# Kernel tuning notes

Measured on AMD Instinct MI355X. Metric: run time of the kernel, lower is better.

Reference implementation:

```python
import jax, jax.numpy as jnp
import numpy as np

EPS = 1e-5

def _conv3x3(x, w, b):
    y = jax.lax.conv_general_dilated(x, w, window_strides=(1, 1),
                                     padding=((1, 1), (1, 1)),
                                     dimension_numbers=('NCHW', 'OIHW', 'NCHW'))
    return y + b[None, :, None, None]

def _bilinear_gather(x, py, px):
    # x: [B,C,H,W]; py,px: [B,K,H,W] absolute sampling coords; zero outside image (DCN convention).
    B, C, H, W = x.shape
    Kk = py.shape[1]
    y0 = jnp.floor(py)
    x0 = jnp.floor(px)
    ly = py - y0
    lx = px - x0
    y0i = y0.astype(jnp.int32)
    x0i = x0.astype(jnp.int32)
    xf = x.reshape(B, C, H * W)

    def gather(yi, xi):
        valid = (yi >= 0) & (yi < H) & (xi >= 0) & (xi < W)
        idx = (jnp.clip(yi, 0, H - 1) * W + jnp.clip(xi, 0, W - 1)).reshape(B, -1)
        g = jax.vmap(lambda xb, ib: xb[:, ib])(xf, idx).reshape(B, C, Kk, H, W)
        return g * valid[:, None].astype(x.dtype)

    v00 = gather(y0i, x0i)
    v01 = gather(y0i, x0i + 1)
    v10 = gather(y0i + 1, x0i)
    v11 = gather(y0i + 1, x0i + 1)
    ly = ly[:, None]
    lx = lx[:, None]
    return (v00 * (1 - ly) * (1 - lx) + v01 * (1 - ly) * lx
            + v10 * ly * (1 - lx) + v11 * ly * lx)

def _shift_forward(x, w_off, b_off, w_conv, b_conv, gamma, beta, run_mean, run_var):
    B, C, H, W = x.shape
    om = _conv3x3(x, w_off, b_off)              # [B,27,H,W] offset/mask predictor
    dy = om[:, 0:18:2]                          # [B,9,H,W] per-tap y offsets
    dx = om[:, 1:18:2]                          # [B,9,H,W] per-tap x offsets
    mask = jax.nn.sigmoid(om[:, 18:27])         # [B,9,H,W] modulation (DCNv2)
    kk = jnp.arange(3, dtype=x.dtype) - 1.0     # kernel tap offsets for 3x3, dilation 1
    ky = jnp.repeat(kk, 3)                      # [9]
    kx = jnp.tile(kk, 3)                        # [9]
    hh = jnp.arange(H, dtype=x.dtype)
    ww = jnp.arange(W, dtype=x.dtype)
    py = hh[None, None, :, None] + ky[None, :, None, None] + dy
    px = ww[None, None, None, :] + kx[None, :, None, None] + dx
    s = _bilinear_gather(x, py, px) * mask[:, None]   # [B,C,9,H,W]
    Co = w_conv.shape[0]
    y = jnp.einsum('bckhw,ock->bohw', s, w_conv.reshape(Co, C, 9))
    y = y + b_conv[None, :, None, None]
    # BatchNorm2d (inference) + ReLU, then residual add
    inv = jax.lax.rsqrt(run_var + EPS)
    y = (y - run_mean[None, :, None, None]) * (inv * gamma)[None, :, None, None] + beta[None, :, None, None]
    y = jax.nn.relu(y)
    return x + y

def setup_inputs():
    key = jax.random.key(0)
    ks = jax.random.split(key, 3)
    B, C, H, W = 2, 256, 96, 96
    x = jax.random.normal(ks[0], (B, C, H, W), dtype=jnp.float32)
    w_off = jax.random.normal(ks[1], (27, C, 3, 3), dtype=jnp.float32) * 0.01
    b_off = jnp.zeros((27,), dtype=jnp.float32)
    w_conv = jax.random.normal(ks[2], (C, C, 3, 3), dtype=jnp.float32) * 0.02
    b_conv = jnp.zeros((C,), dtype=jnp.float32)
    gamma = jnp.ones((C,), dtype=jnp.float32)
    beta = jnp.zeros((C,), dtype=jnp.float32)
    run_mean = jnp.zeros((C,), dtype=jnp.float32)
    run_var = jnp.ones((C,), dtype=jnp.float32)
    return {"x": x, "w_off": w_off, "b_off": b_off, "w_conv": w_conv,
            "b_conv": b_conv, "gamma": gamma, "beta": beta,
            "run_mean": run_mean, "run_var": run_var}

def reference(x, w_off, b_off, w_conv, b_conv, gamma, beta, run_mean, run_var):
    return _shift_forward(x, w_off, b_off, w_conv, b_conv, gamma, beta, run_mean, run_var)
```

## Files before the change

kernel.cpp:

```cpp
#include <hip/hip_runtime.h>
#include <hip/hip_bf16.h>

#define H_ 96
#define W_ 96
#define HW_ 9216
#define C_ 256
#define B_ 2
#define KO_ 27
#define NPX_ 18432
#define EPS_ 1e-5f

typedef unsigned short u16;
typedef unsigned short ushort8 __attribute__((ext_vector_type(8)));
typedef short short8v __attribute__((ext_vector_type(8)));
typedef float float4v __attribute__((ext_vector_type(4)));

__device__ __forceinline__ float b2f(u16 u) {
    return __uint_as_float(((unsigned int)u) << 16);
}
__device__ __forceinline__ u16 f2b(float f) {
    __hip_bfloat16 h = __float2bfloat16(f);
    union { __hip_bfloat16 h; u16 u; } cv; cv.h = h; return cv.u;
}
__device__ __forceinline__ unsigned int pack2(float a, float b) {
    union { __hip_bfloat162 h; unsigned int u; } cv;
    cv.h = __float22bfloat162_rn(make_float2(a, b));
    return cv.u;
}
__device__ __forceinline__ void glds16(const u16* g, u16* l) {
    __builtin_amdgcn_global_load_lds(
        (const __attribute__((address_space(1))) void*)g,
        (__attribute__((address_space(3))) void*)l, 16, 0, 0);
}

__global__ __launch_bounds__(256) void prep_w_kernel(
    const float* __restrict__ w_conv, const float* __restrict__ w_off,
    const float* __restrict__ b_conv,
    const float* __restrict__ gamma, const float* __restrict__ beta,
    const float* __restrict__ rmean, const float* __restrict__ rvar,
    float* __restrict__ AB, u16* __restrict__ WQ, u16* __restrict__ WO)
{
    if (blockIdx.x == 0) {
        int o = threadIdx.x;
        float sc = gamma[o] * rsqrtf(rvar[o] + EPS_);
        AB[o] = sc;
        AB[256 + o] = beta[o] + (b_conv[o] - rmean[o]) * sc;
    }
    if (blockIdx.x < 2304) {
        int idx = blockIdx.x * 256 + threadIdx.x;
        int ch = idx >> 13;
        int o  = (idx >> 5) & 255;
        int cpa = idx & 31;
        int cp  = cpa ^ ((o & 3) << 3);
        int c  = ((ch & 7) << 5) + cp;
        int k  = ch >> 3;
        WQ[idx] = f2b(w_conv[(o * C_ + c) * 9 + k]);
    } else {
        int j = (blockIdx.x - 2304) * 256 + threadIdx.x;
        int ch = j >> 10;
        int o  = (j >> 5) & 31;
        int cp = j & 31;
        int c  = ((ch & 7) << 5) + cp;
        int k  = ch >> 3;
        WO[j] = (o < KO_) ? f2b(w_off[(o * C_ + c) * 9 + k]) : (u16)0;
    }
}

__global__ __launch_bounds__(256) void xt_kernel(const float* __restrict__ x,
                                                 u16* __restrict__ XT)
{
    __shared__ u16 ls[32][100];
    int h  = blockIdx.x;
    int cg = blockIdx.y & 7;
    int b  = blockIdx.y >> 3;
    int c0 = cg * 32;
    for (int e = threadIdx.x; e < 32 * W_; e += 256) {
        int ci = e / W_, w = e % W_;
        ls[ci][w] = f2b(x[((b * C_ + c0 + ci) * H_ + h) * W_ + w]);
    }
    __syncthreads();
    for (int e = threadIdx.x; e < 32 * W_; e += 256) {
        int w = e >> 5, ci = e & 31;
        XT[((b * H_ + h) * W_ + w) * C_ + c0 + ci] = ls[ci][w];
    }
}

__global__ __launch_bounds__(256) void offsets_kernel(
    const u16* __restrict__ XT, const u16* __restrict__ WO,
    const float* __restrict__ b_off, float* __restrict__ OFF)
{
    __shared__ float red[4][32][16];

    const int tid = threadIdx.x;
    const int b  = blockIdx.y;
    const int p0 = blockIdx.x * 16;
    const int h  = p0 / W_;
    const int w0 = p0 % W_;

    const int wave = tid >> 6;
    const int lane = tid & 63;
    const int quad = lane >> 4;
    const int l15  = lane & 15;

    {
        const int pw = w0 + l15;
        float4v acc0 = float4v{0.f,0.f,0.f,0.f};
        float4v acc1 = float4v{0.f,0.f,0.f,0.f};
        int basec = 0; bool vld = true; int curtap = -1;
        auto set_tap = [&](int tap) {
            int py  = h + tap / 3 - 1;
            int pxl = pw + tap % 3 - 1;
            vld = ((unsigned)py < (unsigned)H_) && ((unsigned)pxl < (unsigned)W_);
            int pyc = min(max(py, 0), H_ - 1);
            int pxc = min(max(pxl, 0), W_ - 1);
            basec = ((b * H_ + pyc) * W_ + pxc) * C_ + quad * 8;
        };
        auto bload = [&](int c32) -> ushort8 {
            ushort8 v = *(const ushort8*)(XT + basec + (c32 & 7) * 32);
#pragma unroll
            for (int j = 0; j < 8; j++) v[j] = vld ? v[j] : (u16)0;
            return v;
        };
        const int c0 = wave * 18, c1 = c0 + 18;
        curtap = c0 >> 3;
        set_tap(curtap);
        ushort8 bq = bload(c0);
        short8v wa = *(const short8v*)(WO + c0 * 1024 + l15 * 32 + quad * 8);
        short8v wb = *(const short8v*)(WO + c0 * 1024 + l15 * 32 + quad * 8 + 512);
        for (int i = c0; i < c1; ++i) {
            ushort8 bc = bq;
            short8v wac = wa, wbc = wb;
            int nx = i + 1;
            if (nx < c1) {
                int t = nx >> 3;
                if (t != curtap) { set_tap(t); curtap = t; }
                bq = bload(nx);
                wa = *(const short8v*)(WO + nx * 1024 + l15 * 32 + quad * 8);
                wb = *(const short8v*)(WO + nx * 1024 + l15 * 32 + quad * 8 + 512);
            }
            union { ushort8 u; short8v s; } cb; cb.u = bc;
            acc0 = __builtin_amdgcn_mfma_f32_16x16x32_bf16(wac, cb.s, acc0, 0, 0, 0);
            acc1 = __builtin_amdgcn_mfma_f32_16x16x32_bf16(wbc, cb.s, acc1, 0, 0, 0);
        }
#pragma unroll
        for (int r = 0; r < 4; ++r) {
            red[wave][quad * 4 + r][l15]      = acc0[r];
            red[wave][16 + quad * 4 + r][l15] = acc1[r];
        }
    }
    __syncthreads();
    const int n_base = b * HW_ + p0;
#pragma unroll
    for (int rep = 0; rep < 2; ++rep) {
        int o  = (tid >> 4) + rep * 16;
        int px = tid & 15;
        if (o < KO_) {
            float v = red[0][o][px] + red[1][o][px] + red[2][o][px] + red[3][o][px]
                    + b_off[o];
            OFF[(size_t)(n_base + px) * 32 + o] =
                (o < 18) ? v : 1.f / (1.f + expf(-v));
        }
    }
}

__global__ __launch_bounds__(256) void fused_kernel(
    const float* __restrict__ x, const u16* __restrict__ XT,
    const float* __restrict__ OFF, const u16* __restrict__ WQ,
    const float* __restrict__ AB, float* __restrict__ out)
{
    __shared__ __align__(16) u16 sA[16384];
    __shared__ __align__(16) u16 sB[2048];
    __shared__ float offv[32][32];

    const int tid = threadIdx.x;
    const int wave = tid >> 6;
    const int lane = tid & 63;
    const int quad = lane >> 4;
    const int l15  = lane & 15;
    const int qx   = (quad ^ (l15 & 3)) << 3;

    const int bid = blockIdx.x;
    const int swz = (bid & 7) * 72 + (bid >> 3);
    const int n0  = swz * 32;
    const int b   = n0 / HW_;
    const int p0  = n0 - b * HW_;
    const int h   = p0 / W_;
    const int w0  = p0 % W_;

    {
        int px = tid >> 3, q4 = (tid & 7) * 4;
        float4 v = *(const float4*)(OFF + (size_t)(n0 + px) * 32 + q4);
        *(float4*)&offv[px][q4] = v;
    }
    __syncthreads();

    float4v acc[4][2];
#pragma unroll
    for (int i = 0; i < 4; i++)
#pragma unroll
        for (int jj = 0; jj < 2; jj++)
            acc[i][jj] = float4v{0.f, 0.f, 0.f, 0.f};

    const int le8 = lane * 8;
    const int wo  = wave * 64;

    const int ppx = tid >> 3;
    const int pj  = tid & 7;
    const int sboff = (pj >> 2) * 1024 + ppx * 32
                    + (((pj & 3) ^ (ppx & 3)) << 3);

    float fn0, fn1, fn2, fn3;
    int a00, a01, a10, a11;

    auto tap_setup = [&](int tap) {
        float dy = offv[ppx][2 * tap];
        float dx = offv[ppx][2 * tap + 1];
        float m  = offv[ppx][18 + tap];
        float py  = (float)(h + tap / 3 - 1) + dy;
        float pxx = (float)(w0 + ppx + tap % 3 - 1) + dx;
        float y0f = floorf(py), x0f = floorf(pxx);
        float ly = py - y0f, lx = pxx - x0f;
        int y0 = (int)y0f, x0i = (int)x0f;
        int y1 = y0 + 1, x1 = x0i + 1;
        bool vy0 = (unsigned)y0 < (unsigned)H_;
        bool vy1 = (unsigned)y1 < (unsigned)H_;
        bool vx0 = (unsigned)x0i < (unsigned)W_;
        bool vx1 = (unsigned)x1 < (unsigned)W_;
        fn0 = (vy0 && vx0) ? (1.f - ly) * (1.f - lx) * m : 0.f;
        fn1 = (vy0 && vx1) ? (1.f - ly) * lx * m : 0.f;
        fn2 = (vy1 && vx0) ? ly * (1.f - lx) * m : 0.f;
        fn3 = (vy1 && vx1) ? ly * lx * m : 0.f;
        int y0c = min(max(y0, 0), H_ - 1), y1c = min(max(y1, 0), H_ - 1);
        int x0c = min(max(x0i, 0), W_ - 1), x1c = min(max(x1, 0), W_ - 1);
        a00 = ((b * H_ + y0c) * W_ + x0c) * C_;
        a01 = ((b * H_ + y0c) * W_ + x1c) * C_;
        a10 = ((b * H_ + y1c) * W_ + x0c) * C_;
        a11 = ((b * H_ + y1c) * W_ + x1c) * C_;
    };

    tap_setup(0);
    float fc0 = fn0, fc1 = fn1, fc2 = fn2, fc3 = fn3;
    ushort8 gc00 = *(const ushort8*)(XT + a00 + pj * 8);
    ushort8 gc01 = *(const ushort8*)(XT + a01 + pj * 8);
    ushort8 gc10 = *(const ushort8*)(XT + a10 + pj * 8);
    ushort8 gc11 = *(const ushort8*)(XT + a11 + pj * 8);
#pragma unroll
    for (int i = 0; i < 8; ++i) {
        int unit = i * 4 + wave;
        int cc = unit >> 4;
        glds16(WQ + (size_t)cc * 8192 + (unit & 15) * 512 + le8,
               &sA[unit * 512]);
    }
    ushort8 gn00{}, gn01{}, gn10{}, gn11{};

#pragma unroll 4
    for (int ch = 0; ch < 36; ++ch) {
        {
            float v[8];
#pragma unroll
            for (int t = 0; t < 8; t++)
                v[t] = fc0 * b2f(gc00[t]) + fc1 * b2f(gc01[t])
                     + fc2 * b2f(gc10[t]) + fc3 * b2f(gc11[t]);
            uint4 sv;
            sv.x = pack2(v[0], v[1]);
            sv.y = pack2(v[2], v[3]);
            sv.z = pack2(v[4], v[5]);
            sv.w = pack2(v[6], v[7]);
            *(uint4*)&sB[sboff] = sv;
        }
        asm volatile("s_waitcnt vmcnt(0) lgkmcnt(0)" ::: "memory");
        __builtin_amdgcn_s_barrier();

        short8v af[2][4], bfr[2][2];
#pragma unroll
        for (int cc = 0; cc < 2; ++cc) {
#pragma unroll
            for (int mt = 0; mt < 4; ++mt)
                af[cc][mt] = *(const short8v*)
                    &sA[cc * 8192 + (wo + mt * 16 + l15) * 32 + qx];
#pragma unroll
            for (int nt = 0; nt < 2; ++nt)
                bfr[cc][nt] = *(const short8v*)
                    &sB[cc * 1024 + (nt * 16 + l15) * 32 + qx];
        }
        asm volatile("s_waitcnt lgkmcnt(0)" ::: "memory");
        __builtin_amdgcn_s_barrier();

        if (ch < 35) {
            const int chn = ch + 1, tapn = chn >> 2, qn = chn & 3;
            if (qn == 0) tap_setup(tapn);
            const int cb = qn * 64 + pj * 8;
            gn00 = *(const ushort8*)(XT + a00 + cb);
            gn01 = *(const ushort8*)(XT + a01 + cb);
            gn10 = *(const ushort8*)(XT + a10 + cb);
            gn11 = *(const ushort8*)(XT + a11 + cb);
#pragma unroll
            for (int i = 0; i < 8; ++i) {
                int unit = i * 4 + wave;
                int cc = unit >> 4;
                glds16(WQ + (size_t)(tapn * 8 + qn * 2 + cc) * 8192
                          + (unit & 15) * 512 + le8,
                       &sA[unit * 512]);
            }
        }
        __builtin_amdgcn_s_setprio(1);
#pragma unroll
        for (int cc = 0; cc < 2; ++cc)
#pragma unroll
            for (int mt = 0; mt < 4; ++mt)
#pragma unroll
                for (int nt = 0; nt < 2; ++nt)
                    acc[mt][nt] = __builtin_amdgcn_mfma_f32_16x16x32_bf16(
                        af[cc][mt], bfr[cc][nt], acc[mt][nt], 0, 0, 0);
        __builtin_amdgcn_s_setprio(0);
        gc00 = gn00; gc01 = gn01; gc10 = gn10; gc11 = gn11;
        fc0 = fn0; fc1 = fn1; fc2 = fn2; fc3 = fn3;
    }

    const float* Ao = AB;
    const float* Bo = AB + 256;
#pragma unroll
    for (int mt = 0; mt < 4; mt++) {
#pragma unroll
        for (int nt = 0; nt < 2; nt++) {
            int pix = p0 + nt * 16 + l15;
#pragma unroll
            for (int r = 0; r < 4; r++) {
                int o = wo + mt * 16 + quad * 4 + r;
                float v = acc[mt][nt][r] * Ao[o] + Bo[o];
                v = fmaxf(v, 0.f);
                int gi = (b * C_ + o) * HW_ + pix;
                out[gi] = x[gi] + v;
            }
        }
    }
}

extern "C" void kernel_launch(void* const* d_in, const int* in_sizes, int n_in,
                              void* d_out, int out_size, void* d_ws, size_t ws_size,
                              hipStream_t stream)
{
    (void)in_sizes; (void)n_in; (void)out_size; (void)ws_size;
    const float* x      = (const float*)d_in[0];
    const float* w_off  = (const float*)d_in[1];
    const float* b_off  = (const float*)d_in[2];
    const float* w_conv = (const float*)d_in[3];
    const float* b_conv = (const float*)d_in[4];
    const float* gamma  = (const float*)d_in[5];
    const float* beta   = (const float*)d_in[6];
    const float* rmean  = (const float*)d_in[7];
    const float* rvar   = (const float*)d_in[8];
    float* out = (float*)d_out;

    float* ws = (float*)d_ws;
    float* AB = ws;
    u16* WQ = (u16*)(AB + 512);
    u16* WO = WQ + 589824;
    u16* XT = WO + 73728;
    float* OFF = (float*)(XT + 4718592);

    prep_w_kernel<<<2592, 256, 0, stream>>>(w_conv, w_off, b_conv, gamma, beta,
                                            rmean, rvar, AB, WQ, WO);
    xt_kernel<<<dim3(96, 16), 256, 0, stream>>>(x, XT);
    offsets_kernel<<<dim3(576, 2), 256, 0, stream>>>(XT, WO, b_off, OFF);
    fused_kernel<<<576, 256, 0, stream>>>(x, XT, OFF, WQ, AB, out);
}
```

Measured before the change: 177.6 us.

## Fuse offset predictor into main kernel and merge prep launches; load weights directly

```diff
diff --git a/kernel.cpp b/kernel.cpp
--- a/kernel.cpp
+++ b/kernel.cpp
@@ -12,6 +12,7 @@
 
 typedef unsigned short u16;
 typedef unsigned short ushort8 __attribute__((ext_vector_type(8)));
+typedef unsigned short ushort4v __attribute__((ext_vector_type(4)));
 typedef short short8v __attribute__((ext_vector_type(8)));
 typedef float float4v __attribute__((ext_vector_type(4)));
 
@@ -27,157 +28,77 @@
     cv.h = __float22bfloat162_rn(make_float2(a, b));
     return cv.u;
 }
-__device__ __forceinline__ void glds16(const u16* g, u16* l) {
-    __builtin_amdgcn_global_load_lds(
-        (const __attribute__((address_space(1))) void*)g,
-        (__attribute__((address_space(3))) void*)l, 16, 0, 0);
-}
-
-__global__ __launch_bounds__(256) void prep_w_kernel(
+
+__global__ __launch_bounds__(256) void prep_kernel(
+    const float* __restrict__ x,
     const float* __restrict__ w_conv, const float* __restrict__ w_off,
     const float* __restrict__ b_conv,
     const float* __restrict__ gamma, const float* __restrict__ beta,
     const float* __restrict__ rmean, const float* __restrict__ rvar,
-    float* __restrict__ AB, u16* __restrict__ WQ, u16* __restrict__ WO)
+    float* __restrict__ AB, u16* __restrict__ WQ, u16* __restrict__ WO,
+    u16* __restrict__ XT)
 {
-    if (blockIdx.x == 0) {
-        int o = threadIdx.x;
-        float sc = gamma[o] * rsqrtf(rvar[o] + EPS_);
-        AB[o] = sc;
-        AB[256 + o] = beta[o] + (b_conv[o] - rmean[o]) * sc;
-    }
-    if (blockIdx.x < 2304) {
-        int idx = blockIdx.x * 256 + threadIdx.x;
+    __shared__ u16 ls[32][100];
+    const int bx = blockIdx.x;
+    if (bx < 2304) {
+        if (bx == 0) {
+            int o = threadIdx.x;
+            float sc = gamma[o] * rsqrtf(rvar[o] + EPS_);
+            AB[o] = sc;
+            AB[256 + o] = beta[o] + (b_conv[o] - rmean[o]) * sc;
+        }
+        int idx = bx * 256 + threadIdx.x;
         int ch = idx >> 13;
         int o  = (idx >> 5) & 255;
-        int cpa = idx & 31;
-        int cp  = cpa ^ ((o & 3) << 3);
+        int cp = idx & 31;
         int c  = ((ch & 7) << 5) + cp;
         int k  = ch >> 3;
         WQ[idx] = f2b(w_conv[(o * C_ + c) * 9 + k]);
-    } else {
-        int j = (blockIdx.x - 2304) * 256 + threadIdx.x;
+    } else if (bx < 2592) {
+        int j = (bx - 2304) * 256 + threadIdx.x;
         int ch = j >> 10;
         int o  = (j >> 5) & 31;
         int cp = j & 31;
         int c  = ((ch & 7) << 5) + cp;
         int k  = ch >> 3;
         WO[j] = (o < KO_) ? f2b(w_off[(o * C_ + c) * 9 + k]) : (u16)0;
-    }
-}
-
-__global__ __launch_bounds__(256) void xt_kernel(const float* __restrict__ x,
-                                                 u16* __restrict__ XT)
+    } else {
+        int bid = bx - 2592;
+        int h  = bid % 96;
+        int by = bid / 96;
+        int cg = by & 7;
+        int b  = by >> 3;
+        int c0 = cg * 32;
+        for (int e = threadIdx.x; e < 32 * W_; e += 256) {
+            int ci = e / W_, w = e % W_;
+            ls[ci][w] = f2b(x[((b * C_ + c0 + ci) * H_ + h) * W_ + w]);
+        }
+        __syncthreads();
+        for (int u = threadIdx.x; u < 768; u += 256) {
+            int g4 = u & 7, w = u >> 3;
+            ushort4v v;
+#pragma unroll
+            for (int t = 0; t < 4; t++) v[t] = ls[g4 * 4 + t][w];
+            *(ushort4v*)&XT[((b * H_ + h) * W_ + w) * C_ + c0 + g4 * 4] = v;
+        }
+    }
+}
+
+__global__ __launch_bounds__(256) void fused_kernel(
+    const float* __restrict__ x, const u16* __restrict__ XT,
+    const u16* __restrict__ WO, const float* __restrict__ b_off,
+    const u16* __restrict__ WQ, const float* __restrict__ AB,
+    float* __restrict__ out)
 {
-    __shared__ u16 ls[32][100];
-    int h  = blockIdx.x;
-    int cg = blockIdx.y & 7;
-    int b  = blockIdx.y >> 3;
-    int c0 = cg * 32;
-    for (int e = threadIdx.x; e < 32 * W_; e += 256) {
-        int ci = e / W_, w = e % W_;
-        ls[ci][w] = f2b(x[((b * C_ + c0 + ci) * H_ + h) * W_ + w]);
-    }
-    __syncthreads();
-    for (int e = threadIdx.x; e < 32 * W_; e += 256) {
-        int w = e >> 5, ci = e & 31;
-        XT[((b * H_ + h) * W_ + w) * C_ + c0 + ci] = ls[ci][w];
-    }
-}
-
-__global__ __launch_bounds__(256) void offsets_kernel(
-    const u16* __restrict__ XT, const u16* __restrict__ WO,
-    const float* __restrict__ b_off, float* __restrict__ OFF)
-{
-    __shared__ float red[4][32][16];
-
-    const int tid = threadIdx.x;
-    const int b  = blockIdx.y;
-    const int p0 = blockIdx.x * 16;
-    const int h  = p0 / W_;
-    const int w0 = p0 % W_;
-
+    __shared__ float red[4][2][32][17];
+    __shared__ __align__(16) u16 sB[2048];
+    __shared__ float offv[32][36];
+
+    const int tid  = threadIdx.x;
     const int wave = tid >> 6;
     const int lane = tid & 63;
     const int quad = lane >> 4;
     const int l15  = lane & 15;
-
-    {
-        const int pw = w0 + l15;
-        float4v acc0 = float4v{0.f,0.f,0.f,0.f};
-        float4v acc1 = float4v{0.f,0.f,0.f,0.f};
-        int basec = 0; bool vld = true; int curtap = -1;
-        auto set_tap = [&](int tap) {
-            int py  = h + tap / 3 - 1;
-            int pxl = pw + tap % 3 - 1;
-            vld = ((unsigned)py < (unsigned)H_) && ((unsigned)pxl < (unsigned)W_);
-            int pyc = min(max(py, 0), H_ - 1);
-            int pxc = min(max(pxl, 0), W_ - 1);
-            basec = ((b * H_ + pyc) * W_ + pxc) * C_ + quad * 8;
-        };
-        auto bload = [&](int c32) -> ushort8 {
-            ushort8 v = *(const ushort8*)(XT + basec + (c32 & 7) * 32);
-#pragma unroll
-            for (int j = 0; j < 8; j++) v[j] = vld ? v[j] : (u16)0;
-            return v;
-        };
-        const int c0 = wave * 18, c1 = c0 + 18;
-        curtap = c0 >> 3;
-        set_tap(curtap);
-        ushort8 bq = bload(c0);
-        short8v wa = *(const short8v*)(WO + c0 * 1024 + l15 * 32 + quad * 8);
-        short8v wb = *(const short8v*)(WO + c0 * 1024 + l15 * 32 + quad * 8 + 512);
-        for (int i = c0; i < c1; ++i) {
-            ushort8 bc = bq;
-            short8v wac = wa, wbc = wb;
-            int nx = i + 1;
-            if (nx < c1) {
-                int t = nx >> 3;
-                if (t != curtap) { set_tap(t); curtap = t; }
-                bq = bload(nx);
-                wa = *(const short8v*)(WO + nx * 1024 + l15 * 32 + quad * 8);
-                wb = *(const short8v*)(WO + nx * 1024 + l15 * 32 + quad * 8 + 512);
-            }
-            union { ushort8 u; short8v s; } cb; cb.u = bc;
-            acc0 = __builtin_amdgcn_mfma_f32_16x16x32_bf16(wac, cb.s, acc0, 0, 0, 0);
-            acc1 = __builtin_amdgcn_mfma_f32_16x16x32_bf16(wbc, cb.s, acc1, 0, 0, 0);
-        }
-#pragma unroll
-        for (int r = 0; r < 4; ++r) {
-            red[wave][quad * 4 + r][l15]      = acc0[r];
-            red[wave][16 + quad * 4 + r][l15] = acc1[r];
-        }
-    }
-    __syncthreads();
-    const int n_base = b * HW_ + p0;
-#pragma unroll
-    for (int rep = 0; rep < 2; ++rep) {
-        int o  = (tid >> 4) + rep * 16;
-        int px = tid & 15;
-        if (o < KO_) {
-            float v = red[0][o][px] + red[1][o][px] + red[2][o][px] + red[3][o][px]
-                    + b_off[o];
-            OFF[(size_t)(n_base + px) * 32 + o] =
-                (o < 18) ? v : 1.f / (1.f + expf(-v));
-        }
-    }
-}
-
-__global__ __launch_bounds__(256) void fused_kernel(
-    const float* __restrict__ x, const u16* __restrict__ XT,
-    const float* __restrict__ OFF, const u16* __restrict__ WQ,
-    const float* __restrict__ AB, float* __restrict__ out)
-{
-    __shared__ __align__(16) u16 sA[16384];
-    __shared__ __align__(16) u16 sB[2048];
-    __shared__ float offv[32][32];
-
-    const int tid = threadIdx.x;
-    const int wave = tid >> 6;
-    const int lane = tid & 63;
-    const int quad = lane >> 4;
-    const int l15  = lane & 15;
-    const int qx   = (quad ^ (l15 & 3)) << 3;
 
     const int bid = blockIdx.x;
     const int swz = (bid & 7) * 72 + (bid >> 3);
@@ -188,9 +109,82 @@
     const int w0  = p0 % W_;
 
     {
-        int px = tid >> 3, q4 = (tid & 7) * 4;
-        float4 v = *(const float4*)(OFF + (size_t)(n0 + px) * 32 + q4);
-        *(float4*)&offv[px][q4] = v;
+        float4v oa[2][2];
+#pragma unroll
+        for (int ph = 0; ph < 2; ph++)
+#pragma unroll
+            for (int hh = 0; hh < 2; hh++)
+                oa[ph][hh] = float4v{0.f, 0.f, 0.f, 0.f};
+
+        int basec0 = 0, basec1 = 0; bool vld0 = true, vld1 = true;
+        auto oset = [&](int tap) {
+            int py = h + tap / 3 - 1;
+            bool vy = (unsigned)py < (unsigned)H_;
+            int pyc = min(max(py, 0), H_ - 1);
+            int rowb = (b * H_ + pyc) * W_;
+            {
+                int pxl = w0 + l15 + tap % 3 - 1;
+                vld0 = vy && ((unsigned)pxl < (unsigned)W_);
+                basec0 = (rowb + min(max(pxl, 0), W_ - 1)) * C_ + quad * 8;
+            }
+            {
+                int pxl = w0 + 16 + l15 + tap % 3 - 1;
+                vld1 = vy && ((unsigned)pxl < (unsigned)W_);
+                basec1 = (rowb + min(max(pxl, 0), W_ - 1)) * C_ + quad * 8;
+            }
+        };
+        auto bld0 = [&](int c32) -> ushort8 {
+            ushort8 v = *(const ushort8*)(XT + basec0 + (c32 & 7) * 32);
+#pragma unroll
+            for (int j = 0; j < 8; j++) v[j] = vld0 ? v[j] : (u16)0;
+            return v;
+        };
+        auto bld1 = [&](int c32) -> ushort8 {
+            ushort8 v = *(const ushort8*)(XT + basec1 + (c32 & 7) * 32);
+#pragma unroll
+            for (int j = 0; j < 8; j++) v[j] = vld1 ? v[j] : (u16)0;
+            return v;
+        };
+        const int i0 = wave * 18, i1 = i0 + 18;
+        int curtap = i0 >> 3;
+        oset(curtap);
+        ushort8 b0 = bld0(i0), b1 = bld1(i0);
+        short8v wa = *(const short8v*)(WO + i0 * 1024 + l15 * 32 + quad * 8);
+        short8v wb = *(const short8v*)(WO + i0 * 1024 + l15 * 32 + quad * 8 + 512);
+        for (int i = i0; i < i1; ++i) {
+            ushort8 c0v = b0, c1v = b1;
+            short8v wac = wa, wbc = wb;
+            int nx = i + 1;
+            if (nx < i1) {
+                int t = nx >> 3;
+                if (t != curtap) { oset(t); curtap = t; }
+                b0 = bld0(nx); b1 = bld1(nx);
+                wa = *(const short8v*)(WO + nx * 1024 + l15 * 32 + quad * 8);
+                wb = *(const short8v*)(WO + nx * 1024 + l15 * 32 + quad * 8 + 512);
+            }
+            union { ushort8 u; short8v s; } u0, u1; u0.u = c0v; u1.u = c1v;
+            oa[0][0] = __builtin_amdgcn_mfma_f32_16x16x32_bf16(wac, u0.s, oa[0][0], 0, 0, 0);
+            oa[0][1] = __builtin_amdgcn_mfma_f32_16x16x32_bf16(wbc, u0.s, oa[0][1], 0, 0, 0);
+            oa[1][0] = __builtin_amdgcn_mfma_f32_16x16x32_bf16(wac, u1.s, oa[1][0], 0, 0, 0);
+            oa[1][1] = __builtin_amdgcn_mfma_f32_16x16x32_bf16(wbc, u1.s, oa[1][1], 0, 0, 0);
+        }
+#pragma unroll
+        for (int r = 0; r < 4; ++r) {
+            red[wave][0][quad * 4 + r][l15]      = oa[0][0][r];
+            red[wave][0][16 + quad * 4 + r][l15] = oa[0][1][r];
+            red[wave][1][quad * 4 + r][l15]      = oa[1][0][r];
+            red[wave][1][16 + quad * 4 + r][l15] = oa[1][1][r];
+        }
+    }
+    __syncthreads();
+    for (int u = tid; u < 1024; u += 256) {
+        int px = u & 31, o = u >> 5;
+        if (o < KO_) {
+            int ph = px >> 4, pp = px & 15;
+            float v = red[0][ph][o][pp] + red[1][ph][o][pp]
+                    + red[2][ph][o][pp] + red[3][ph][o][pp] + b_off[o];
+            offv[px][o] = (o < 18) ? v : 1.f / (1.f + expf(-v));
+        }
     }
     __syncthreads();
 
@@ -201,15 +195,13 @@
         for (int jj = 0; jj < 2; jj++)
             acc[i][jj] = float4v{0.f, 0.f, 0.f, 0.f};
 
-    const int le8 = lane * 8;
     const int wo  = wave * 64;
-
     const int ppx = tid >> 3;
     const int pj  = tid & 7;
-    const int sboff = (pj >> 2) * 1024 + ppx * 32
-                    + (((pj & 3) ^ (ppx & 3)) << 3);
-
-    float fn0, fn1, fn2, fn3;
+    const int sboff = (pj >> 2) * 1024 + ppx * 32 + (((pj & 3) ^ (ppx & 3)) << 3);
+    const int bslot = (quad ^ (l15 & 3)) << 3;
+
+    float fc0, fc1, fc2, fc3, fn0, fn1, fn2, fn3;
     int a00, a01, a10, a11;
 
     auto tap_setup = [&](int tap) {
@@ -239,22 +231,26 @@
     };
 
     tap_setup(0);
-    float fc0 = fn0, fc1 = fn1, fc2 = fn2, fc3 = fn3;
+    fc0 = fn0; fc1 = fn1; fc2 = fn2; fc3 = fn3;
     ushort8 gc00 = *(const ushort8*)(XT + a00 + pj * 8);
     ushort8 gc01 = *(const ushort8*)(XT + a01 + pj * 8);
     ushort8 gc10 = *(const ushort8*)(XT + a10 + pj * 8);
     ushort8 gc11 = *(const ushort8*)(XT + a11 + pj * 8);
-#pragma unroll
-    for (int i = 0; i < 8; ++i) {
-        int unit = i * 4 + wave;
-        int cc = unit >> 4;
-        glds16(WQ + (size_t)cc * 8192 + (unit & 15) * 512 + le8,
-               &sA[unit * 512]);
-    }
     ushort8 gn00{}, gn01{}, gn10{}, gn11{};
 
-#pragma unroll 4
+#pragma unroll 1
     for (int ch = 0; ch < 36; ++ch) {
+        const int tap = ch >> 2, q = ch & 3;
+
+        short8v af[2][4];
+        const u16* wq0 = WQ + (size_t)(tap * 8 + q * 2) * 8192
+                       + (wo + l15) * 32 + quad * 8;
+#pragma unroll
+        for (int cc = 0; cc < 2; ++cc)
+#pragma unroll
+            for (int mt = 0; mt < 4; ++mt)
+                af[cc][mt] = *(const short8v*)(wq0 + cc * 8192 + mt * 512);
+
         {
             float v[8];
 #pragma unroll
@@ -268,23 +264,6 @@
             sv.w = pack2(v[6], v[7]);
             *(uint4*)&sB[sboff] = sv;
         }
-        asm volatile("s_waitcnt vmcnt(0) lgkmcnt(0)" ::: "memory");
-        __builtin_amdgcn_s_barrier();
-
-        short8v af[2][4], bfr[2][2];
-#pragma unroll
-        for (int cc = 0; cc < 2; ++cc) {
-#pragma unroll
-            for (int mt = 0; mt < 4; ++mt)
-                af[cc][mt] = *(const short8v*)
-                    &sA[cc * 8192 + (wo + mt * 16 + l15) * 32 + qx];
-#pragma unroll
-            for (int nt = 0; nt < 2; ++nt)
-                bfr[cc][nt] = *(const short8v*)
-                    &sB[cc * 1024 + (nt * 16 + l15) * 32 + qx];
-        }
-        asm volatile("s_waitcnt lgkmcnt(0)" ::: "memory");
-        __builtin_amdgcn_s_barrier();
 
         if (ch < 35) {
             const int chn = ch + 1, tapn = chn >> 2, qn = chn & 3;
@@ -294,15 +273,23 @@
             gn01 = *(const ushort8*)(XT + a01 + cb);
             gn10 = *(const ushort8*)(XT + a10 + cb);
             gn11 = *(const ushort8*)(XT + a11 + cb);
-#pragma unroll
-            for (int i = 0; i < 8; ++i) {
-                int unit = i * 4 + wave;
-                int cc = unit >> 4;
-                glds16(WQ + (size_t)(tapn * 8 + qn * 2 + cc) * 8192
-                          + (unit & 15) * 512 + le8,
-                       &sA[unit * 512]);
-            }
-        }
+        }
+
+        asm volatile("s_waitcnt lgkmcnt(0)" ::: "memory");
+        __builtin_amdgcn_s_barrier();
+
+        short8v bfr[2][2];
+#pragma unroll
+        for (int cc = 0; cc < 2; ++cc)
+#pragma unroll
+            for (int nt = 0; nt < 2; ++nt)
+                bfr[cc][nt] = *(const short8v*)
+                    &sB[cc * 1024 + (nt * 16 + l15) * 32 + bslot];
+
+        asm volatile("s_waitcnt lgkmcnt(0)" ::: "memory");
+        __builtin_amdgcn_s_barrier();
+        __builtin_amdgcn_sched_barrier(0);
+
         __builtin_amdgcn_s_setprio(1);
 #pragma unroll
         for (int cc = 0; cc < 2; ++cc)
@@ -313,6 +300,7 @@
                     acc[mt][nt] = __builtin_amdgcn_mfma_f32_16x16x32_bf16(
                         af[cc][mt], bfr[cc][nt], acc[mt][nt], 0, 0, 0);
         __builtin_amdgcn_s_setprio(0);
+
         gc00 = gn00; gc01 = gn01; gc10 = gn10; gc11 = gn11;
         fc0 = fn0; fc1 = fn1; fc2 = fn2; fc3 = fn3;
     }
@@ -357,11 +345,8 @@
     u16* WQ = (u16*)(AB + 512);
     u16* WO = WQ + 589824;
     u16* XT = WO + 73728;
-    float* OFF = (float*)(XT + 4718592);
-
-    prep_w_kernel<<<2592, 256, 0, stream>>>(w_conv, w_off, b_conv, gamma, beta,
-                                            rmean, rvar, AB, WQ, WO);
-    xt_kernel<<<dim3(96, 16), 256, 0, stream>>>(x, XT);
-    offsets_kernel<<<dim3(576, 2), 256, 0, stream>>>(XT, WO, b_off, OFF);
-    fused_kernel<<<576, 256, 0, stream>>>(x, XT, OFF, WQ, AB, out);
-}
+
+    prep_kernel<<<4128, 256, 0, stream>>>(x, w_conv, w_off, b_conv, gamma, beta,
+                                          rmean, rvar, AB, WQ, WO, XT);
+    fused_kernel<<<576, 256, 0, stream>>>(x, XT, WO, b_off, WQ, AB, out);
+}
```

Result: no change. 175.0 us (-1.5%).
